# Optimization experiments

Measured on AMD Instinct MI355X. Metric: run time of the kernel, lower is better.

## Reference

```python
import jax, jax.numpy as jnp
import numpy as np

N = 100000
E = 1600000
BN_EPS = 1e-5


def setup_inputs() -> dict:
    key = jax.random.key(0)
    ks = jax.random.split(key, 32)
    rn = lambda k, shape, s=0.05: jax.random.normal(k, shape, jnp.float32) * s
    inp = {
        "x": jax.random.normal(ks[0], (N, 2), jnp.float32),
        "edge_index": jax.random.randint(ks[1], (2, E), 0, N, dtype=jnp.int64),
        # GIN conv1 mlp: Linear(1,256) -> BN(256) -> ReLU -> Linear(256,128)
        "w1": rn(ks[2], (1, 256)), "b1": rn(ks[3], (256,)),
        "g1": jax.random.uniform(ks[4], (256,), jnp.float32, 0.5, 1.5),
        "be1": rn(ks[5], (256,)),
        "m1": rn(ks[6], (256,)),
        "v1": jax.random.uniform(ks[7], (256,), jnp.float32, 0.5, 1.5),
        "w2": rn(ks[8], (256, 128)), "b2": rn(ks[9], (128,)),
        # GIN conv2 mlp: Linear(128,64) -> BN(64) -> ReLU -> Linear(64,64)
        "w3": rn(ks[10], (128, 64)), "b3": rn(ks[11], (64,)),
        "g2": jax.random.uniform(ks[12], (64,), jnp.float32, 0.5, 1.5),
        "be2": rn(ks[13], (64,)),
        "m2": rn(ks[14], (64,)),
        "v2": jax.random.uniform(ks[15], (64,), jnp.float32, 0.5, 1.5),
        # Bilinear(64, 64, 96)
        "wb": rn(ks[16], (96, 64, 64)), "bb": rn(ks[17], (96,)),
        # linear3: 96 -> 6
        "w5": rn(ks[18], (96, 6)), "b5": rn(ks[19], (6,)),
        # linear2: 6 -> 6
        "w6": rn(ks[20], (6, 6)), "b6": rn(ks[21], (6,)),
    }
    return inp


def reference(x, edge_index, w1, b1, g1, be1, m1, v1, w2, b2,
              w3, b3, g2, be2, m2, v2, w4_unused=None, wb=None, bb=None,
              w5=None, b5=None, w6=None, b6=None):
    # note: kept signature explicit below; see _reference
    raise NotImplementedError


def _bn(h, g, b, m, v):
    # inference-mode batchnorm with running stats
    return (h - m) * jax.lax.rsqrt(v + BN_EPS) * g + b


def reference(x, edge_index, w1, b1, g1, be1, m1, v1, w2, b2,
              w3, b3, g2, be2, m2, v2, wb, bb, w5, b5, w6, b6):
    src, dst = edge_index[0], edge_index[1]
    n = x.shape[0]

    def agg(h):
        # GIN sum aggregation: (1+eps)*x + sum_{j in N(i)} x_j, eps=0
        return h + jax.ops.segment_sum(h[src], dst, num_segments=n)

    def block(col):  # col: [n, 1]
        h = agg(col)
        h = jnp.maximum(_bn(h @ w1 + b1, g1, be1, m1, v1), 0.0) @ w2 + b2  # [n,128]
        h = agg(h)
        h = jnp.maximum(_bn(h @ w3 + b3, g2, be2, m2, v2), 0.0)            # mlp2 ends with BN+ReLU? no:
        return h

    # mlp2 = Linear(128,64)->BN(64)->ReLU->Linear(64,64); rebuild correctly inline:
    def block2(col):
        h = agg(col)
        h = jnp.maximum(_bn(h @ w1 + b1, g1, be1, m1, v1), 0.0) @ w2 + b2  # [n,128]
        h = agg(h)
        h = jnp.maximum(_bn(h @ w3 + b3, g2, be2, m2, v2), 0.0)
        return h

    h1 = block2(x[:, 1:2])  # column tmp-1 = 1 first
    h2 = block2(x[:, 0:1])  # then column 0
    # mlp2's final Linear(64,64) is folded below? No -- apply final linear of mlp2:
    # (handled in block2 already via w3 only; second linear uses separate weights)
    hb = jnp.einsum('ni,kij,nj->nk', h1, wb, h2) + bb  # Bilinear(64,64,96)
    h = jnp.maximum(hb @ w5 + b5, 0.0)                 # relu(linear3)
    h = h @ w6 + b6                                    # linear2
    return jax.nn.log_softmax(h, axis=1)
```

## Files before the change

kernel.cpp:

```cpp
#include <hip/hip_runtime.h>
#include <hip/hip_bf16.h>

#define NN 100000
#define NE 1600000
#define EPS 1e-5f
#define NCHUNK 98
#define NB 196
#define BCAP2 10240
#define RND 4096
#define NRND 391

typedef __attribute__((ext_vector_type(8))) short short8;
typedef __attribute__((ext_vector_type(4))) float f32x4;

__device__ __forceinline__ float b2f_lo(unsigned u){ return __uint_as_float(u << 16); }
__device__ __forceinline__ float b2f_hi(unsigned u){ return __uint_as_float(u & 0xffff0000u); }
__device__ __forceinline__ float b2f_u(unsigned short u){ return __uint_as_float(((unsigned)u) << 16); }
__device__ __forceinline__ unsigned short f2b(float f){
  __hip_bfloat16 h = __float2bfloat16(f);
  return __builtin_bit_cast(unsigned short, h);
}

__global__ void k_probe(const int* __restrict__ ei32, int* __restrict__ flag, int* __restrict__ gcur){
  __shared__ int cnt;
  if (threadIdx.x == 0) cnt = 0;
  __syncthreads();
  if (ei32[threadIdx.x * 2 + 1] == 0) atomicAdd(&cnt, 1);
  __syncthreads();
  if (threadIdx.x == 0) flag[0] = (cnt > 200) ? 1 : 0;
  for (int i = threadIdx.x; i < NB; i += 256) gcur[i] = i * BCAP2;
}

__global__ __launch_bounds__(1024) void k_bin(const void* __restrict__ ei, const int* __restrict__ flag,
                                              int* __restrict__ gcur, int* __restrict__ staged){
  __shared__ int hcnt[256];
  __shared__ int pref[256];
  __shared__ int bnd[200];
  __shared__ int hrun[196];
  __shared__ int gb[196];
  __shared__ int sbuf[RND];
  int t = threadIdx.x;
  int base = blockIdx.x * RND;
  bool f64 = (flag[0] != 0);
  int pay[4], bkt[4];
  #pragma unroll
  for (int k = 0; k < 4; ++k){
    int e = base + k * 1024 + t;
    if (e < NE){
      int src, dst;
      if (f64){ src = (int)((const long long*)ei)[e]; dst = (int)((const long long*)ei)[NE + e]; }
      else    { src = ((const int*)ei)[e];            dst = ((const int*)ei)[NE + e]; }
      pay[k] = (src << 9) | (dst & 511);
      bkt[k] = dst >> 9;
    } else { pay[k] = 0; bkt[k] = -1; }
  }
  if (t < 256) hcnt[t] = 0;
  __syncthreads();
  #pragma unroll
  for (int k = 0; k < 4; ++k)
    if (bkt[k] >= 0) atomicAdd(&hcnt[bkt[k]], 1);
  __syncthreads();
  if (t < 256) pref[t] = hcnt[t];
  __syncthreads();
  for (int off = 1; off < 256; off <<= 1){
    int v = 0;
    if (t < 256 && t >= off) v = pref[t - off];
    __syncthreads();
    if (t < 256) pref[t] += v;
    __syncthreads();
  }
  if (t < 196){
    int excl = pref[t] - hcnt[t];
    bnd[t] = excl;
    hrun[t] = excl;
    gb[t] = (hcnt[t] > 0) ? atomicAdd(&gcur[t], hcnt[t]) : 0;
  }
  if (t == 196) bnd[196] = 0;
  __syncthreads();
  if (t == 0) bnd[196] = pref[255];
  __syncthreads();
  #pragma unroll
  for (int k = 0; k < 4; ++k)
    if (bkt[k] >= 0){
      int lp = atomicAdd(&hrun[bkt[k]], 1);
      sbuf[lp] = pay[k];
    }
  __syncthreads();
  int total = bnd[196];
  for (int i = t; i < total; i += 1024){
    int b = 0;
    #pragma unroll
    for (int sh = 128; sh > 0; sh >>= 1)
      if (b + sh <= 196 && bnd[b + sh] <= i) b += sh;
    staged[gb[b] + (i - bnd[b])] = sbuf[i];
  }
}

__global__ __launch_bounds__(256) void k_bdeg(const int* __restrict__ staged, const int* __restrict__ gcur,
                                              int* __restrict__ deg){
  __shared__ int dcnt[512];
  int b = blockIdx.x, t = threadIdx.x;
  for (int l = t; l < 512; l += 256) dcnt[l] = 0;
  __syncthreads();
  int cnt = min(gcur[b] - b * BCAP2, BCAP2);
  const int* sp = staged + b * BCAP2;
  for (int i = t; i < cnt; i += 256)
    atomicAdd(&dcnt[sp[i] & 511], 1);
  __syncthreads();
  for (int l = t; l < 512; l += 256){
    int n = b * 512 + l;
    if (n < NN) deg[n] = dcnt[l];
  }
}

__global__ void k_scan1(const int* __restrict__ deg, int* __restrict__ cinc, int* __restrict__ part){
  __shared__ int b[1024];
  int i = blockIdx.x * 1024 + threadIdx.x;
  int v = (i < NN) ? deg[i] : 0;
  b[threadIdx.x] = v; __syncthreads();
  for (int off = 1; off < 1024; off <<= 1){
    int t = (threadIdx.x >= off) ? b[threadIdx.x - off] : 0;
    __syncthreads();
    b[threadIdx.x] += t;
    __syncthreads();
  }
  if (i < NN) cinc[i] = b[threadIdx.x];
  if (threadIdx.x == 1023) part[blockIdx.x] = b[1023];
}

__global__ void k_scan2(int* __restrict__ part, int nchunk){
  __shared__ int b[128];
  int tid = threadIdx.x;
  int v = (tid < nchunk) ? part[tid] : 0;
  b[tid] = v; __syncthreads();
  for (int off = 1; off < 128; off <<= 1){
    int t = (tid >= off) ? b[tid - off] : 0;
    __syncthreads();
    b[tid] += t;
    __syncthreads();
  }
  if (tid < nchunk) part[tid] = b[tid] - v;
}

__global__ void k_scan3(const int* __restrict__ deg, const int* __restrict__ cinc,
                        const int* __restrict__ part, int* __restrict__ rowp){
  int i = blockIdx.x * 1024 + threadIdx.x;
  if (i < NN){
    rowp[i] = cinc[i] - deg[i] + part[blockIdx.x];
  }
  if (i == 0) rowp[NN] = NE;
}

__global__ __launch_bounds__(256) void k_scatter2(const int* __restrict__ staged, const int* __restrict__ gcur,
                                                  const int* __restrict__ rowp, int* __restrict__ colidx){
  __shared__ int cur[512];
  int b = blockIdx.x, t = threadIdx.x;
  for (int l = t; l < 512; l += 256){
    int n = b * 512 + l;
    cur[l] = (n < NN) ? rowp[n] : 0;
  }
  __syncthreads();
  int cnt = min(gcur[b] - b * BCAP2, BCAP2);
  const int* sp = staged + b * BCAP2;
  for (int i = t; i < cnt; i += 256){
    int p = sp[i];
    int pos = atomicAdd(&cur[p & 511], 1);
    colidx[pos] = p >> 9;
  }
}

__global__ void k_prep_sort(const float* __restrict__ w1, const float* __restrict__ b1,
                            const float* __restrict__ g1, const float* __restrict__ be1,
                            const float* __restrict__ m1, const float* __restrict__ v1,
                            const float* __restrict__ w3, const float* __restrict__ b3,
                            const float* __restrict__ g2, const float* __restrict__ be2,
                            const float* __restrict__ m2, const float* __restrict__ v2,
                            float* __restrict__ aC, float* __restrict__ cC,
                            float* __restrict__ thrS, int* __restrict__ pos,
                            unsigned short* __restrict__ w3s, float* __restrict__ b3p){
  __shared__ float key[256];
  __shared__ int idx[256];
  int tid = threadIdx.x;
  {
    float inv = rsqrtf(v1[tid] + EPS);
    float sc = g1[tid] * inv;
    float a = w1[tid] * sc;
    float c = (b1[tid] - m1[tid]) * sc + be1[tid];
    aC[tid] = a; cC[tid] = c;
    key[tid] = (a != 0.0f) ? (-c / a) : __int_as_float(0x7f800000);
    idx[tid] = tid;
  }
  __syncthreads();
  for (int k = 2; k <= 256; k <<= 1){
    for (int j = k >> 1; j > 0; j >>= 1){
      int ixj = tid ^ j;
      if (ixj > tid){
        float k1 = key[tid], k2 = key[ixj];
        bool asc = ((tid & k) == 0);
        if ((k1 > k2) == asc){
          int i1 = idx[tid];
          key[tid] = k2; key[ixj] = k1;
          idx[tid] = idx[ixj]; idx[ixj] = i1;
        }
      }
      __syncthreads();
    }
  }
  thrS[tid] = key[tid];
  pos[idx[tid]] = tid;
  if (tid < 64){
    float i2 = rsqrtf(v2[tid] + EPS);
    b3p[tid] = (b3[tid] - m2[tid]) * i2 * g2[tid] + be2[tid];
  }
  for (int id = tid; id < 8192; id += 256){
    int cs = id >> 11, r = id & 2047;
    int kt = r >> 9;  r &= 511;
    int l = r >> 3;   int mi = r & 7;
    int krow = kt * 32 + (l >> 4) * 8 + mi;
    int col  = cs * 16 + (l & 15);
    float i2 = rsqrtf(v2[col] + EPS);
    w3s[id] = f2b(w3[krow * 64 + col] * i2 * g2[col]);
  }
}

__global__ void k_tab(const float* __restrict__ aC, const float* __restrict__ cC,
                      const int* __restrict__ pos, const float* __restrict__ w2,
                      const float* __restrict__ b2, unsigned short* __restrict__ tabG){
  __shared__ float ca[256], cc[256];
  int t = blockIdx.x;
  int tid = threadIdx.x;
  {
    float a = aC[tid], c = cC[tid];
    int p = pos[tid];
    bool act = (a > 0.f) ? (p < t) : ((a < 0.f) ? (p >= t) : (c > 0.f));
    ca[tid] = act ? a : 0.f;
    cc[tid] = act ? c : 0.f;
  }
  __syncthreads();
  int f = tid & 127, sel = tid >> 7;
  const float* coef = sel ? cc : ca;
  float acc = sel ? b2[f] : 0.f;
  #pragma unroll 8
  for (int j = 0; j < 256; ++j)
    acc = fmaf(coef[j], w2[j * 128 + f], acc);
  tabG[t * 256 + sel * 128 + f] = f2b(acc);
}

__global__ void k_wbS(const float* __restrict__ wb, unsigned short* __restrict__ wbS){
  int id = blockIdx.x * 256 + threadIdx.x;
  if (id >= 64 * 6144) return;
  int j = id / 6144;
  int r = id % 6144;
  int f = r >> 9;  r &= 511;
  int l = r >> 3;  int mi = r & 7;
  int kt = f / 6, cs = f % 6;
  int i = kt * 32 + (l >> 4) * 8 + mi;
  int k = cs * 16 + (l & 15);
  wbS[id] = f2b(wb[(k * 64 + i) * 64 + j]);
}

__global__ void k_sagg(const float* __restrict__ x, const int* __restrict__ rowp,
                       const int* __restrict__ colidx, const float* __restrict__ thrS,
                       float4* __restrict__ info){
  __shared__ float thr[256];
  thr[threadIdx.x] = thrS[threadIdx.x];
  __syncthreads();
  int n = blockIdx.x * 256 + threadIdx.x;
  if (n >= NN) return;
  float2 xv = ((const float2*)x)[n];
  float sA = xv.y, sB = xv.x;
  int s0 = rowp[n], s1 = rowp[n + 1];
  for (int e = s0; e < s1; ++e){
    int j = colidx[e];
    float2 xj = ((const float2*)x)[j];
    sA += xj.y; sB += xj.x;
  }
  int tA = 0, tB = 0;
  #pragma unroll
  for (int sh = 128; sh > 0; sh >>= 1){
    if (tA + sh <= 256 && thr[tA + sh - 1] < sA) tA += sh;
    if (tB + sh <= 256 && thr[tB + sh - 1] < sB) tB += sh;
  }
  info[n] = make_float4(sA, sB, __uint_as_float((unsigned)tA | ((unsigned)tB << 16)), 0.f);
}

__global__ __launch_bounds__(1024) void k_agg(
    const float4* __restrict__ info, const int* __restrict__ rowp,
    const int* __restrict__ colidx, const unsigned short* __restrict__ tabG,
    unsigned short* __restrict__ mA, unsigned short* __restrict__ mB){
  extern __shared__ unsigned tab32[];
  for (int i = threadIdx.x; i < 257 * 128; i += 1024)
    tab32[i] = ((const unsigned*)tabG)[i];
  __syncthreads();
  int lane = threadIdx.x & 63;
  int wv = (blockIdx.x * 1024 + threadIdx.x) >> 6;
  int nw = (gridDim.x * 1024) >> 6;
  int p  = lane >> 5;
  int fq = lane & 31;
  for (int n = wv; n < NN; n += nw){
    int s0 = rowp[n], cnt = rowp[n + 1] - s0 + 1;
    float a0 = 0.f, a1 = 0.f, a2 = 0.f, a3 = 0.f;
    for (int base = 0; base < cnt; base += 64){
      int nb = base + lane;
      float4 inf;
      if (nb < cnt){
        int j = (nb == 0) ? n : colidx[s0 + nb - 1];
        inf = info[j];
      } else inf = make_float4(0, 0, 0, 0);
      int m = min(cnt - base, 64);
      for (int q = 0; q < m; ++q){
        float sA = __shfl(inf.x, q);
        float sB = __shfl(inf.y, q);
        unsigned tt = __float_as_uint(__shfl(inf.z, q));
        float s = p ? sB : sA;
        int   t = p ? (int)(tt >> 16) : (int)(tt & 0xffffu);
        const unsigned* rp = &tab32[t * 128];
        uint2 av = *(const uint2*)&rp[fq * 2];
        uint2 bv = *(const uint2*)&rp[64 + fq * 2];
        a0 += fmaf(s, b2f_lo(av.x), b2f_lo(bv.x));
        a1 += fmaf(s, b2f_hi(av.x), b2f_hi(bv.x));
        a2 += fmaf(s, b2f_lo(av.y), b2f_lo(bv.y));
        a3 += fmaf(s, b2f_hi(av.y), b2f_hi(bv.y));
      }
    }
    unsigned short* dst = (p ? mB : mA) + n * 128 + fq * 4;
    unsigned o0 = (unsigned)f2b(a0) | ((unsigned)f2b(a1) << 16);
    unsigned o1 = (unsigned)f2b(a2) | ((unsigned)f2b(a3) << 16);
    *((uint2*)dst) = make_uint2(o0, o1);
  }
}

__global__ void k_mlp2(const unsigned short* __restrict__ mA, const unsigned short* __restrict__ mB,
                       const unsigned short* __restrict__ w3s, const float* __restrict__ b3p,
                       unsigned short* __restrict__ h1, unsigned short* __restrict__ h2T){
  int lane = threadIdx.x & 63;
  int tile = (blockIdx.x * blockDim.x + threadIdx.x) >> 6;
  const int NT = 2 * NN / 16;
  if (tile >= NT) return;
  bool pB = (tile >= NN / 16);
  const unsigned short* src = pB ? (mB + (size_t)(tile - NN / 16) * 16 * 128)
                                 : (mA + (size_t)tile * 16 * 128);
  short8 afr[4];
  {
    int row = lane & 15, ko = (lane >> 4) * 8;
    #pragma unroll
    for (int kt = 0; kt < 4; ++kt)
      afr[kt] = *(const short8*)(src + row * 128 + kt * 32 + ko);
  }
  f32x4 acc[4];
  #pragma unroll
  for (int cs = 0; cs < 4; ++cs){
    f32x4 a = {0.f, 0.f, 0.f, 0.f};
    #pragma unroll
    for (int kt = 0; kt < 4; ++kt){
      short8 b = *(const short8*)(w3s + ((cs * 4 + kt) * 64 + lane) * 8);
      a = __builtin_amdgcn_mfma_f32_16x16x32_bf16(afr[kt], b, a, 0, 0, 0);
    }
    acc[cs] = a;
  }
  int col0 = lane & 15, r0 = (lane >> 4) * 4;
  if (!pB){
    int nb = tile * 16;
    #pragma unroll
    for (int cs = 0; cs < 4; ++cs){
      float bias = b3p[cs * 16 + col0];
      #pragma unroll
      for (int r = 0; r < 4; ++r){
        float v = fmaxf(acc[cs][r] + bias, 0.f);
        h1[(size_t)(nb + r0 + r) * 64 + cs * 16 + col0] = f2b(v);
      }
    }
  } else {
    int nb = (tile - NN / 16) * 16;
    #pragma unroll
    for (int cs = 0; cs < 4; ++cs){
      float bias = b3p[cs * 16 + col0];
      unsigned p0 = (unsigned)f2b(fmaxf(acc[cs][0] + bias, 0.f)) | ((unsigned)f2b(fmaxf(acc[cs][1] + bias, 0.f)) << 16);
      unsigned p1 = (unsigned)f2b(fmaxf(acc[cs][2] + bias, 0.f)) | ((unsigned)f2b(fmaxf(acc[cs][3] + bias, 0.f)) << 16);
      *(uint2*)(h2T + (size_t)(cs * 16 + col0) * NN + nb + r0) = make_uint2(p0, p1);
    }
  }
}

__global__ __launch_bounds__(128, 2) void k_bil(
    const unsigned short* __restrict__ h1, const unsigned short* __restrict__ h2T,
    const unsigned short* __restrict__ wbS, const float* __restrict__ bbv,
    const float* __restrict__ w5, const float* __restrict__ b5,
    const float* __restrict__ w6, const float* __restrict__ b6,
    float* __restrict__ out){
  __shared__ float smem[3136];
  unsigned short* h2sT = (unsigned short*)smem;
  int tid = threadIdx.x;
  int lane = tid & 63;
  int wv = tid >> 6;
  int nb = blockIdx.x * 64;
  int rl = lane & 15, ko = (lane >> 4) * 8;
  for (int i = tid; i < 64 * 64; i += 128){
    int j = i >> 6, l = (i >> 2) & 15, rt = i & 3;
    int n = nb + rt * 16 + l;
    h2sT[i] = (n < NN) ? h2T[(size_t)j * NN + n] : (unsigned short)0;
  }
  float af[4][2][8];
  #pragma unroll
  for (int rt = 0; rt < 4; ++rt){
    int row = nb + rt * 16 + rl;
    #pragma unroll
    for (int kt = 0; kt < 2; ++kt){
      if (row < NN){
        uint4 rv = *(const uint4*)(h1 + (size_t)row * 64 + kt * 32 + ko);
        af[rt][kt][0] = b2f_lo(rv.x); af[rt][kt][1] = b2f_hi(rv.x);
        af[rt][kt][2] = b2f_lo(rv.y); af[rt][kt][3] = b2f_hi(rv.y);
        af[rt][kt][4] = b2f_lo(rv.z); af[rt][kt][5] = b2f_hi(rv.z);
        af[rt][kt][6] = b2f_lo(rv.w); af[rt][kt][7] = b2f_hi(rv.w);
      } else {
        #pragma unroll
        for (int e = 0; e < 8; ++e) af[rt][kt][e] = 0.f;
      }
    }
  }
  __syncthreads();
  f32x4 acc[4][6];
  #pragma unroll
  for (int rt = 0; rt < 4; ++rt)
    #pragma unroll
    for (int cs = 0; cs < 6; ++cs)
      acc[rt][cs] = (f32x4){0.f, 0.f, 0.f, 0.f};
  const unsigned short* wp = wbS + (size_t)lane * 8;
  int j0 = wv * 32, j1 = j0 + 32;
  for (int j = j0; j < j1; ++j){
    uint4 bf[2][6];
    #pragma unroll
    for (int kt = 0; kt < 2; ++kt)
      #pragma unroll
      for (int cs = 0; cs < 6; ++cs)
        bf[kt][cs] = *(const uint4*)(wp + (size_t)(j * 12 + kt * 6 + cs) * 512);
    uint2 hsv = *(const uint2*)(h2sT + j * 64 + rl * 4);
    float hsr[4];
    hsr[0] = b2f_lo(hsv.x); hsr[1] = b2f_hi(hsv.x);
    hsr[2] = b2f_lo(hsv.y); hsr[3] = b2f_hi(hsv.y);
    #pragma unroll
    for (int rt = 0; rt < 4; ++rt){
      float hs = hsr[rt];
      short8 a0, a1;
      #pragma unroll
      for (int e = 0; e < 8; ++e){
        a0[e] = (short)f2b(af[rt][0][e] * hs);
        a1[e] = (short)f2b(af[rt][1][e] * hs);
      }
      #pragma unroll
      for (int cs = 0; cs < 6; ++cs){
        acc[rt][cs] = __builtin_amdgcn_mfma_f32_16x16x32_bf16(a0, __builtin_bit_cast(short8, bf[0][cs]), acc[rt][cs], 0, 0, 0);
        acc[rt][cs] = __builtin_amdgcn_mfma_f32_16x16x32_bf16(a1, __builtin_bit_cast(short8, bf[1][cs]), acc[rt][cs], 0, 0, 0);
      }
    }
  }
  float* red = smem;
  __syncthreads();
  if (wv == 1){
    #pragma unroll
    for (int rt = 0; rt < 4; ++rt)
      #pragma unroll
      for (int cs = 0; cs < 3; ++cs){
        int col = cs * 16 + rl;
        #pragma unroll
        for (int r = 0; r < 4; ++r){
          int row = rt * 16 + (lane >> 4) * 4 + r;
          red[row * 49 + col] = acc[rt][cs][r];
        }
      }
  }
  __syncthreads();
  if (wv == 0){
    #pragma unroll
    for (int rt = 0; rt < 4; ++rt)
      #pragma unroll
      for (int cs = 0; cs < 3; ++cs){
        int col = cs * 16 + rl;
        #pragma unroll
        for (int r = 0; r < 4; ++r){
          int row = rt * 16 + (lane >> 4) * 4 + r;
          acc[rt][cs][r] += red[row * 49 + col];
        }
      }
  }
  __syncthreads();
  if (wv == 1){
    #pragma unroll
    for (int rt = 0; rt < 4; ++rt)
      #pragma unroll
      for (int cs = 3; cs < 6; ++cs){
        int col = (cs - 3) * 16 + rl;
        #pragma unroll
        for (int r = 0; r < 4; ++r){
          int row = rt * 16 + (lane >> 4) * 4 + r;
          red[row * 49 + col] = acc[rt][cs][r];
        }
      }
  }
  __syncthreads();
  if (wv == 0){
    #pragma unroll
    for (int rt = 0; rt < 4; ++rt)
      #pragma unroll
      for (int cs = 3; cs < 6; ++cs){
        int col = (cs - 3) * 16 + rl;
        #pragma unroll
        for (int r = 0; r < 4; ++r){
          int row = rt * 16 + (lane >> 4) * 4 + r;
          acc[rt][cs][r] += red[row * 49 + col];
        }
      }
  }
  __syncthreads();
  if (wv == 0){
    unsigned short* hbs = (unsigned short*)smem;
    #pragma unroll
    for (int rt = 0; rt < 4; ++rt)
      #pragma unroll
      for (int cs = 0; cs < 6; ++cs){
        int col = cs * 16 + rl;
        float bias = bbv[col];
        #pragma unroll
        for (int r = 0; r < 4; ++r){
          int rowl = rt * 16 + (lane >> 4) * 4 + r;
          hbs[rowl * 98 + col] = f2b(acc[rt][cs][r] + bias);
        }
      }
    int n = nb + lane;
    if (n < NN){
      float u[6];
      #pragma unroll
      for (int q = 0; q < 6; ++q) u[q] = b5[q];
      for (int jj = 0; jj < 96; ++jj){
        float hv = b2f_u(hbs[lane * 98 + jj]);
        #pragma unroll
        for (int q = 0; q < 6; ++q) u[q] = fmaf(hv, w5[jj * 6 + q], u[q]);
      }
      #pragma unroll
      for (int q = 0; q < 6; ++q) u[q] = fmaxf(u[q], 0.f);
      float v[6];
      #pragma unroll
      for (int q = 0; q < 6; ++q){
        float a2 = b6[q];
        #pragma unroll
        for (int pp = 0; pp < 6; ++pp) a2 = fmaf(u[pp], w6[pp * 6 + q], a2);
        v[q] = a2;
      }
      float mx = v[0];
      #pragma unroll
      for (int q = 1; q < 6; ++q) mx = fmaxf(mx, v[q]);
      float se = 0.f;
      #pragma unroll
      for (int q = 0; q < 6; ++q) se += expf(v[q] - mx);
      float ls = logf(se);
      #pragma unroll
      for (int q = 0; q < 6; ++q) out[(size_t)n * 6 + q] = v[q] - mx - ls;
    }
  }
}

extern "C" void kernel_launch(void* const* d_in, const int* in_sizes, int n_in,
                              void* d_out, int out_size, void* d_ws, size_t ws_size,
                              hipStream_t stream){
  const float* x   = (const float*)d_in[0];
  const void*  ei  = d_in[1];
  const float* w1  = (const float*)d_in[2];
  const float* b1  = (const float*)d_in[3];
  const float* g1  = (const float*)d_in[4];
  const float* be1 = (const float*)d_in[5];
  const float* m1  = (const float*)d_in[6];
  const float* v1  = (const float*)d_in[7];
  const float* w2  = (const float*)d_in[8];
  const float* b2  = (const float*)d_in[9];
  const float* w3  = (const float*)d_in[10];
  const float* b3  = (const float*)d_in[11];
  const float* g2  = (const float*)d_in[12];
  const float* be2 = (const float*)d_in[13];
  const float* m2  = (const float*)d_in[14];
  const float* v2  = (const float*)d_in[15];
  const float* wb  = (const float*)d_in[16];
  const float* bb  = (const float*)d_in[17];
  const float* w5  = (const float*)d_in[18];
  const float* b5  = (const float*)d_in[19];
  const float* w6  = (const float*)d_in[20];
  const float* b6  = (const float*)d_in[21];
  float* out = (float*)d_out;

  char* ws = (char*)d_ws;
  size_t off = 0;
  auto alloc = [&](size_t bytes) -> void* {
    void* p = ws + off;
    off += (bytes + 255) & ~(size_t)255;
    return p;
  };
  int* deg      = (int*)alloc((size_t)NN * 4);
  int* rowp     = (int*)alloc((size_t)(NN + 1) * 4);
  int* cinc     = (int*)alloc((size_t)NN * 4);
  int* part     = (int*)alloc(1024 * 4);
  int* flag     = (int*)alloc(256);
  int* gcur     = (int*)alloc((size_t)NB * 4 + 256);
  int* colidx   = (int*)alloc((size_t)NE * 4);
  float4* info  = (float4*)alloc((size_t)NN * 16);
  unsigned short* tabG = (unsigned short*)alloc(257 * 256 * 2);
  float* thrS   = (float*)alloc(256 * 4);
  float* aC     = (float*)alloc(256 * 4);
  float* cC     = (float*)alloc(256 * 4);
  int* pos      = (int*)alloc(256 * 4);
  unsigned short* w3s  = (unsigned short*)alloc(8192 * 2);
  float* b3p    = (float*)alloc(64 * 4);
  unsigned short* wbS  = (unsigned short*)alloc((size_t)393216 * 2);
  unsigned short* mA   = (unsigned short*)alloc((size_t)NN * 128 * 2);
  unsigned short* mB   = (unsigned short*)alloc((size_t)NN * 128 * 2);
  unsigned short* h1   = (unsigned short*)alloc((size_t)NN * 64 * 2);
  unsigned short* h2T  = (unsigned short*)alloc((size_t)NN * 64 * 2);
  int* staged   = (int*)mA;

  k_probe<<<1, 256, 0, stream>>>((const int*)ei, flag, gcur);
  k_bin<<<NRND, 1024, 0, stream>>>(ei, flag, gcur, staged);
  k_bdeg<<<NB, 256, 0, stream>>>(staged, gcur, deg);
  k_scan1<<<NCHUNK, 1024, 0, stream>>>(deg, cinc, part);
  k_scan2<<<1, 128, 0, stream>>>(part, NCHUNK);
  k_scan3<<<NCHUNK, 1024, 0, stream>>>(deg, cinc, part, rowp);
  k_scatter2<<<NB, 256, 0, stream>>>(staged, gcur, rowp, colidx);
  k_prep_sort<<<1, 256, 0, stream>>>(w1, b1, g1, be1, m1, v1, w3, b3, g2, be2, m2, v2,
                                     aC, cC, thrS, pos, w3s, b3p);
  k_tab<<<257, 256, 0, stream>>>(aC, cC, pos, w2, b2, tabG);
  k_wbS<<<(64 * 6144 + 255) / 256, 256, 0, stream>>>(wb, wbS);
  k_sagg<<<(NN + 255) / 256, 256, 0, stream>>>(x, rowp, colidx, thrS, info);
  hipFuncSetAttribute((const void*)k_agg, hipFuncAttributeMaxDynamicSharedMemorySize, 257 * 128 * 4);
  k_agg<<<256, 1024, 257 * 128 * 4, stream>>>(info, rowp, colidx, tabG, mA, mB);
  k_mlp2<<<(2 * NN / 16 + 3) / 4, 256, 0, stream>>>(mA, mB, w3s, b3p, h1, h2T);
  k_bil<<<(NN + 63) / 64, 128, 0, stream>>>(h1, h2T, wbS, bb, w5, b5, w6, b6, out);
}
```

Measured before the change: 322.6 us.

## Split k_agg feature dimension across block pairs to halve LDS table size

Each k_agg block now loads only half of the 128-feature lookup table into LDS (64 words per threshold row instead of 128), and the grid is doubled so odd and even blocks each handle one half of the output features. The goal is to cut per-block shared memory from about 131KB to about 66KB, letting more blocks sit on a CU, and to shrink per-lane LDS reads and accumulators. In exchange, every node's neighbor list, info gathers and shuffles are done twice, once per feature half.

```diff
diff --git a/kernel.cpp b/kernel.cpp
--- a/kernel.cpp
+++ b/kernel.cpp
@@ -286,20 +286,24 @@
 
 __global__ __launch_bounds__(1024) void k_agg(
     const float4* __restrict__ info, const int* __restrict__ rowp,
-    const int* __restrict__ colidx, const unsigned short* __restrict__ tabG,
+    const int* __restrict__ colidx, const unsigned* __restrict__ tabG32,
     unsigned short* __restrict__ mA, unsigned short* __restrict__ mB){
-  extern __shared__ unsigned tab32[];
-  for (int i = threadIdx.x; i < 257 * 128; i += 1024)
-    tab32[i] = ((const unsigned*)tabG)[i];
+  extern __shared__ unsigned tabH[];
+  int hb = blockIdx.x & 1;
+  for (int i = threadIdx.x; i < 257 * 64; i += 1024){
+    int t = i >> 6, w = i & 63;
+    int srcw = t * 128 + hb * 32 + w + ((w >= 32) ? 32 : 0);
+    tabH[i] = tabG32[srcw];
+  }
   __syncthreads();
   int lane = threadIdx.x & 63;
-  int wv = (blockIdx.x * 1024 + threadIdx.x) >> 6;
-  int nw = (gridDim.x * 1024) >> 6;
+  int wv = ((blockIdx.x >> 1) * 1024 + threadIdx.x) >> 6;
+  int nw = (gridDim.x >> 1) << 4;
   int p  = lane >> 5;
   int fq = lane & 31;
   for (int n = wv; n < NN; n += nw){
     int s0 = rowp[n], cnt = rowp[n + 1] - s0 + 1;
-    float a0 = 0.f, a1 = 0.f, a2 = 0.f, a3 = 0.f;
+    float a0 = 0.f, a1 = 0.f;
     for (int base = 0; base < cnt; base += 64){
       int nb = base + lane;
       float4 inf;
@@ -314,19 +318,14 @@
         unsigned tt = __float_as_uint(__shfl(inf.z, q));
         float s = p ? sB : sA;
         int   t = p ? (int)(tt >> 16) : (int)(tt & 0xffffu);
-        const unsigned* rp = &tab32[t * 128];
-        uint2 av = *(const uint2*)&rp[fq * 2];
-        uint2 bv = *(const uint2*)&rp[64 + fq * 2];
-        a0 += fmaf(s, b2f_lo(av.x), b2f_lo(bv.x));
-        a1 += fmaf(s, b2f_hi(av.x), b2f_hi(bv.x));
-        a2 += fmaf(s, b2f_lo(av.y), b2f_lo(bv.y));
-        a3 += fmaf(s, b2f_hi(av.y), b2f_hi(bv.y));
-      }
-    }
-    unsigned short* dst = (p ? mB : mA) + n * 128 + fq * 4;
-    unsigned o0 = (unsigned)f2b(a0) | ((unsigned)f2b(a1) << 16);
-    unsigned o1 = (unsigned)f2b(a2) | ((unsigned)f2b(a3) << 16);
-    *((uint2*)dst) = make_uint2(o0, o1);
+        unsigned av = tabH[t * 64 + fq];
+        unsigned bv = tabH[t * 64 + 32 + fq];
+        a0 += fmaf(s, b2f_lo(av), b2f_lo(bv));
+        a1 += fmaf(s, b2f_hi(av), b2f_hi(bv));
+      }
+    }
+    unsigned short* dst = (p ? mB : mA) + (size_t)n * 128 + hb * 64 + fq * 2;
+    *((unsigned*)dst) = (unsigned)f2b(a0) | ((unsigned)f2b(a1) << 16);
   }
 }
 
@@ -627,8 +626,8 @@
   k_tab<<<257, 256, 0, stream>>>(aC, cC, pos, w2, b2, tabG);
   k_wbS<<<(64 * 6144 + 255) / 256, 256, 0, stream>>>(wb, wbS);
   k_sagg<<<(NN + 255) / 256, 256, 0, stream>>>(x, rowp, colidx, thrS, info);
-  hipFuncSetAttribute((const void*)k_agg, hipFuncAttributeMaxDynamicSharedMemorySize, 257 * 128 * 4);
-  k_agg<<<256, 1024, 257 * 128 * 4, stream>>>(info, rowp, colidx, tabG, mA, mB);
+  hipFuncSetAttribute((const void*)k_agg, hipFuncAttributeMaxDynamicSharedMemorySize, 257 * 64 * 4);
+  k_agg<<<512, 1024, 257 * 64 * 4, stream>>>(info, rowp, colidx, (const unsigned*)tabG, mA, mB);
   k_mlp2<<<(2 * NN / 16 + 3) / 4, 256, 0, stream>>>(mA, mB, w3s, b3p, h1, h2T);
   k_bil<<<(NN + 63) / 64, 128, 0, stream>>>(h1, h2T, wbS, bb, w5, b5, w6, b6, out);
 }
```

Result: slower. 370.0 us (+14.7%).

## Materialize per-node MLP1 outputs then gather-sum instead of recomputing per edge

Applied to the files above, without the earlier changes.

The fused aggregation recomputed each neighbour's 128-wide MLP1 output from the shared-memory lookup table on every edge. It is replaced by a kernel that evaluates each node's output once into a bf16 buffer, and a second kernel that gathers and sums those rows over the CSR neighbours, with two edges per wavefront. This turns per-edge table arithmetic into plain 256-byte row reads. In exchange it adds an extra global write and read of the intermediate buffer per path, reuses the h1 allocation as scratch, and runs the two paths sequentially.

```diff
diff --git a/kernel.cpp b/kernel.cpp
--- a/kernel.cpp
+++ b/kernel.cpp
@@ -284,49 +284,57 @@
   info[n] = make_float4(sA, sB, __uint_as_float((unsigned)tA | ((unsigned)tB << 16)), 0.f);
 }
 
-__global__ __launch_bounds__(1024) void k_agg(
-    const float4* __restrict__ info, const int* __restrict__ rowp,
-    const int* __restrict__ colidx, const unsigned short* __restrict__ tabG,
-    unsigned short* __restrict__ mA, unsigned short* __restrict__ mB){
-  extern __shared__ unsigned tab32[];
-  for (int i = threadIdx.x; i < 257 * 128; i += 1024)
-    tab32[i] = ((const unsigned*)tabG)[i];
-  __syncthreads();
+__global__ __launch_bounds__(256) void k_y(const float4* __restrict__ info,
+                                           const unsigned* __restrict__ tabG32,
+                                           unsigned* __restrict__ y, int path){
+  int id = blockIdx.x * 256 + threadIdx.x;
+  int n = id >> 5, q = id & 31;
+  if (n >= NN) return;
+  float4 inf = info[n];
+  float s = path ? inf.y : inf.x;
+  unsigned tt = __float_as_uint(inf.z);
+  int t = path ? (int)(tt >> 16) : (int)(tt & 0xffffu);
+  const unsigned* rp = tabG32 + t * 128;
+  uint2 av = *(const uint2*)(rp + 2 * q);
+  uint2 bv = *(const uint2*)(rp + 64 + 2 * q);
+  float v0 = fmaf(s, b2f_lo(av.x), b2f_lo(bv.x));
+  float v1 = fmaf(s, b2f_hi(av.x), b2f_hi(bv.x));
+  float v2 = fmaf(s, b2f_lo(av.y), b2f_lo(bv.y));
+  float v3 = fmaf(s, b2f_hi(av.y), b2f_hi(bv.y));
+  unsigned o0 = (unsigned)f2b(v0) | ((unsigned)f2b(v1) << 16);
+  unsigned o1 = (unsigned)f2b(v2) | ((unsigned)f2b(v3) << 16);
+  *(uint2*)(y + (size_t)n * 64 + 2 * q) = make_uint2(o0, o1);
+}
+
+__global__ __launch_bounds__(256) void k_gather(const unsigned* __restrict__ y,
+                                                const int* __restrict__ rowp,
+                                                const int* __restrict__ colidx,
+                                                unsigned short* __restrict__ mOut){
   int lane = threadIdx.x & 63;
-  int wv = (blockIdx.x * 1024 + threadIdx.x) >> 6;
-  int nw = (gridDim.x * 1024) >> 6;
-  int p  = lane >> 5;
-  int fq = lane & 31;
+  int wv = (blockIdx.x * 256 + threadIdx.x) >> 6;
+  int nw = (gridDim.x * 256) >> 6;
+  int h = lane >> 5, fl = lane & 31;
   for (int n = wv; n < NN; n += nw){
     int s0 = rowp[n], cnt = rowp[n + 1] - s0 + 1;
     float a0 = 0.f, a1 = 0.f, a2 = 0.f, a3 = 0.f;
-    for (int base = 0; base < cnt; base += 64){
-      int nb = base + lane;
-      float4 inf;
-      if (nb < cnt){
-        int j = (nb == 0) ? n : colidx[s0 + nb - 1];
-        inf = info[j];
-      } else inf = make_float4(0, 0, 0, 0);
-      int m = min(cnt - base, 64);
-      for (int q = 0; q < m; ++q){
-        float sA = __shfl(inf.x, q);
-        float sB = __shfl(inf.y, q);
-        unsigned tt = __float_as_uint(__shfl(inf.z, q));
-        float s = p ? sB : sA;
-        int   t = p ? (int)(tt >> 16) : (int)(tt & 0xffffu);
-        const unsigned* rp = &tab32[t * 128];
-        uint2 av = *(const uint2*)&rp[fq * 2];
-        uint2 bv = *(const uint2*)&rp[64 + fq * 2];
-        a0 += fmaf(s, b2f_lo(av.x), b2f_lo(bv.x));
-        a1 += fmaf(s, b2f_hi(av.x), b2f_hi(bv.x));
-        a2 += fmaf(s, b2f_lo(av.y), b2f_lo(bv.y));
-        a3 += fmaf(s, b2f_hi(av.y), b2f_hi(bv.y));
-      }
-    }
-    unsigned short* dst = (p ? mB : mA) + n * 128 + fq * 4;
-    unsigned o0 = (unsigned)f2b(a0) | ((unsigned)f2b(a1) << 16);
-    unsigned o1 = (unsigned)f2b(a2) | ((unsigned)f2b(a3) << 16);
-    *((uint2*)dst) = make_uint2(o0, o1);
+    for (int base = 0; base < cnt; base += 2){
+      int ec = base + h;
+      if (ec < cnt){
+        int j = (ec == 0) ? n : colidx[s0 + ec - 1];
+        uint2 v = *(const uint2*)(y + (size_t)j * 64 + fl * 2);
+        a0 += b2f_lo(v.x); a1 += b2f_hi(v.x);
+        a2 += b2f_lo(v.y); a3 += b2f_hi(v.y);
+      }
+    }
+    a0 += __shfl_xor(a0, 32);
+    a1 += __shfl_xor(a1, 32);
+    a2 += __shfl_xor(a2, 32);
+    a3 += __shfl_xor(a3, 32);
+    if (h == 0){
+      unsigned o0 = (unsigned)f2b(a0) | ((unsigned)f2b(a1) << 16);
+      unsigned o1 = (unsigned)f2b(a2) | ((unsigned)f2b(a3) << 16);
+      *(uint2*)((unsigned*)(mOut + (size_t)n * 128) + fl * 2) = make_uint2(o0, o1);
+    }
   }
 }
 
@@ -614,6 +622,7 @@
   unsigned short* h1   = (unsigned short*)alloc((size_t)NN * 64 * 2);
   unsigned short* h2T  = (unsigned short*)alloc((size_t)NN * 64 * 2);
   int* staged   = (int*)mA;
+  unsigned* y   = (unsigned*)h1;
 
   k_probe<<<1, 256, 0, stream>>>((const int*)ei, flag, gcur);
   k_bin<<<NRND, 1024, 0, stream>>>(ei, flag, gcur, staged);
@@ -627,8 +636,10 @@
   k_tab<<<257, 256, 0, stream>>>(aC, cC, pos, w2, b2, tabG);
   k_wbS<<<(64 * 6144 + 255) / 256, 256, 0, stream>>>(wb, wbS);
   k_sagg<<<(NN + 255) / 256, 256, 0, stream>>>(x, rowp, colidx, thrS, info);
-  hipFuncSetAttribute((const void*)k_agg, hipFuncAttributeMaxDynamicSharedMemorySize, 257 * 128 * 4);
-  k_agg<<<256, 1024, 257 * 128 * 4, stream>>>(info, rowp, colidx, tabG, mA, mB);
+  k_y<<<(NN * 32 + 255) / 256, 256, 0, stream>>>(info, (const unsigned*)tabG, y, 0);
+  k_gather<<<2048, 256, 0, stream>>>(y, rowp, colidx, mA);
+  k_y<<<(NN * 32 + 255) / 256, 256, 0, stream>>>(info, (const unsigned*)tabG, y, 1);
+  k_gather<<<2048, 256, 0, stream>>>(y, rowp, colidx, mB);
   k_mlp2<<<(2 * NN / 16 + 3) / 4, 256, 0, stream>>>(mA, mB, w3s, b3p, h1, h2T);
   k_bil<<<(NN + 63) / 64, 128, 0, stream>>>(h1, h2T, wbS, bb, w5, b5, w6, b6, out);
 }
```

Measured after the change: 449.0 us. 39.2% more time.
